# Optimization experiments

Measured on AMD Instinct MI355X. Metric: run time of the kernel, lower is better.

The kernel has to match this reference:

```python
import jax, jax.numpy as jnp
import numpy as np

D = 8
W = 256
NUM_FREQS = 10
NUM_FREQS_VIEWS = 4
SKIPS = (4,)
PE_DIM = 3 + 2 * 3 * NUM_FREQS        # 63
VE_DIM = 3 + 2 * 3 * NUM_FREQS_VIEWS  # 27
N_RAYS, N_SAMPLES = 4096, 64


def embed(x, num_freqs):
    # torch order: [x, sin(x*f0), cos(x*f0), sin(x*f1), cos(x*f1), ...]
    freqs = (2.0 ** jnp.arange(num_freqs)).astype(x.dtype)
    xf = x[..., None, :] * freqs[:, None]              # [..., F, 3]
    sc = jnp.stack([jnp.sin(xf), jnp.cos(xf)], axis=-2)  # [..., F, 2, 3]
    return jnp.concatenate([x, sc.reshape(*x.shape[:-1], num_freqs * 6)], -1)


def setup_inputs() -> dict:
    key = jax.random.key(0)
    ks = iter(jax.random.split(key, 32))
    inp = {}
    inp["input_pts"] = jax.random.normal(next(ks), (N_RAYS, N_SAMPLES, 3), jnp.float32)
    inp["input_views"] = jax.random.normal(next(ks), (N_RAYS, 3), jnp.float32)
    # pts MLP: layer 5 (index 5) takes W + PE_DIM due to skip after layer 4
    in_dims = [PE_DIM] + [(W + PE_DIM) if i in SKIPS else W for i in range(D - 1)]
    for i, d in enumerate(in_dims):
        inp[f"pts_w{i}"] = jax.random.normal(next(ks), (d, W), jnp.float32) / np.sqrt(d).astype(np.float32)
        inp[f"pts_b{i}"] = jnp.zeros((W,), jnp.float32)
    inp["views_w"] = jax.random.normal(next(ks), (VE_DIM + W, W // 2), jnp.float32) / np.sqrt(VE_DIM + W).astype(np.float32)
    inp["views_b"] = jnp.zeros((W // 2,), jnp.float32)
    inp["feat_w"] = jax.random.normal(next(ks), (W, W), jnp.float32) / np.sqrt(W).astype(np.float32)
    inp["feat_b"] = jnp.zeros((W,), jnp.float32)
    inp["alpha_w"] = jax.random.normal(next(ks), (W, 1), jnp.float32) / np.sqrt(W).astype(np.float32)
    inp["alpha_b"] = jnp.zeros((1,), jnp.float32)
    inp["rgb_w"] = jax.random.normal(next(ks), (W // 2, 3), jnp.float32) / np.sqrt(W // 2).astype(np.float32)
    inp["rgb_b"] = jnp.zeros((3,), jnp.float32)
    return inp


def reference(input_pts, input_views,
              pts_w0, pts_b0, pts_w1, pts_b1, pts_w2, pts_b2, pts_w3, pts_b3,
              pts_w4, pts_b4, pts_w5, pts_b5, pts_w6, pts_b6, pts_w7, pts_b7,
              views_w, views_b, feat_w, feat_b, alpha_w, alpha_b, rgb_w, rgb_b):
    pts_ws = [pts_w0, pts_w1, pts_w2, pts_w3, pts_w4, pts_w5, pts_w6, pts_w7]
    pts_bs = [pts_b0, pts_b1, pts_b2, pts_b3, pts_b4, pts_b5, pts_b6, pts_b7]
    R, S = input_pts.shape[0], input_pts.shape[1]
    ep = embed(input_pts, NUM_FREQS).reshape(-1, PE_DIM)            # [R*S, 63]
    ev = embed(input_views, NUM_FREQS_VIEWS)                        # [R, 27]
    ev = jnp.broadcast_to(ev[:, None, :], (R, S, VE_DIM)).reshape(-1, VE_DIM)
    h = ep
    for i in range(D):
        h = jax.nn.relu(h @ pts_ws[i] + pts_bs[i])
        if i in SKIPS:
            h = jnp.concatenate([ep, h], -1)
    alpha = h @ alpha_w + alpha_b                                    # [R*S, 1]
    feature = h @ feat_w + feat_b                                    # [R*S, W]
    h2 = jax.nn.relu(jnp.concatenate([feature, ev], -1) @ views_w + views_b)
    rgb = h2 @ rgb_w + rgb_b                                         # [R*S, 3]
    return jnp.concatenate([rgb, alpha], -1).reshape(R, S, 4)
```

## Files before the change

kernel.cpp:

```cpp
#include <hip/hip_runtime.h>

typedef _Float16 h16;
typedef __attribute__((ext_vector_type(8))) _Float16 half8;
typedef __attribute__((ext_vector_type(4))) _Float16 half4;
typedef __attribute__((ext_vector_type(4))) float f32x4;
typedef __attribute__((ext_vector_type(16))) float f32x16;

constexpr size_t OFF_P0 = 0;
constexpr size_t OFF_P1 = 16384;
constexpr size_t OFF_P2 = 81920;
constexpr size_t OFF_P3 = 147456;
constexpr size_t OFF_P4 = 212992;
constexpr size_t OFF_P5 = 278528;
constexpr size_t OFF_P6 = 360448;
constexpr size_t OFF_P7 = 425984;
constexpr size_t OFF_FEAT = 491520;
constexpr size_t OFF_VIEWS = 557056;

__device__ __forceinline__ f32x16 mfma32(half8 a, half8 b, f32x16 c) {
  return __builtin_amdgcn_mfma_f32_32x32x16_f16(a, b, c, 0, 0, 0);
}
__device__ __forceinline__ half8 ldfrag(const h16* __restrict__ base, int frag, int l) {
  return *(const half8*)(base + (size_t)frag * 512 + (size_t)l * 8);
}
__device__ __forceinline__ half8 ldsfrag(const h16* __restrict__ base, int frag, int l) {
  return *(const half8*)(base + frag * 512 + l * 8);
}

__global__ void convw_kernel(const float* __restrict__ src, h16* __restrict__ dst,
                             int Ksrc, int N, int Kp, int p, int npad, int rot) {
  int t = blockIdx.x * 256 + threadIdx.x;
  int nfrags = (Kp >> 4) * (N >> 5);
  int frag = t >> 6;
  if (frag >= nfrags) return;
  int l = t & 63;
  int ntiles = N >> 5;
  int kt = frag / ntiles;
  int nt = frag - kt * ntiles;
  int col = nt * 32 + (l & 31);
  int kbase = kt * 16 + (l >> 5) * 8;
  half8 v;
#pragma unroll
  for (int j = 0; j < 8; ++j) {
    int pr = kbase + j + rot;
    if (pr >= Kp) pr -= Kp;
    float x = 0.f;
    if (pr < p) {
      x = src[(size_t)pr * N + col];
    } else if (pr >= p + npad) {
      int r = pr - npad;
      if (r < Ksrc) x = src[(size_t)r * N + col];
    }
    v[j] = (h16)x;
  }
  *(half8*)(dst + (size_t)frag * 512 + (size_t)l * 8) = v;
}

struct Params {
  const float* pts;
  const float* views;
  const h16* wf;
  const float* pb[8];
  const float* views_b;
  const float* feat_b;
  const float* alpha_w;
  const float* alpha_b;
  const float* rgb_w;
  const float* rgb_b;
  float* out;
};

template <bool RELU>
__device__ __forceinline__ void epiW(h16* __restrict__ Y, const f32x16& A,
                                     int rt, int ct, const float* __restrict__ bias,
                                     int lr, int lh) {
#pragma unroll
  for (int g = 0; g < 4; ++g) {
    int col0 = ct * 32 + g * 8 + lh * 4;
    f32x4 bv = *(const f32x4*)(bias + col0);
    half4 pk;
#pragma unroll
    for (int i = 0; i < 4; ++i) {
      float v = A[g * 4 + i] + bv[i];
      if (RELU) v = fmaxf(v, 0.f);
      pk[i] = (h16)v;
    }
    *(half4*)(Y + (rt * 16 + ct * 2 + (g >> 1)) * 512 + ((g & 1) * 32 + lr) * 8 + lh * 4) = pk;
  }
}

template <int KTTOT, int XSTRIDE, bool RELU, bool EXTEP>
__device__ __forceinline__ void layerT(
    const h16* __restrict__ X, const h16* __restrict__ EPb, h16* __restrict__ Y,
    const h16* __restrict__ wcur, const h16* __restrict__ wnext,
    int nstride, int nbA, int nbB, const float* __restrict__ bias,
    half8 (&rA)[4], half8 (&rB)[4], int rp, int ctA, int ctB, int l) {
  const int lr = l & 31, lh = l >> 5;
  f32x16 a00 = (f32x16)0.f, a01 = (f32x16)0.f, a10 = (f32x16)0.f, a11 = (f32x16)0.f;
#pragma unroll
  for (int kt = 0; kt < KTTOT; ++kt) {
    half8 x0, x1;
    if (!EXTEP || kt < 16) {
      x0 = ldsfrag(X, (2 * rp) * XSTRIDE + kt, l);
      x1 = ldsfrag(X, (2 * rp + 1) * XSTRIDE + kt, l);
    } else {
      x0 = ldsfrag(EPb, (2 * rp) * 4 + (kt - 16), l);
      x1 = ldsfrag(EPb, (2 * rp + 1) * 4 + (kt - 16), l);
    }
    half8 bA = rA[kt & 3], bB = rB[kt & 3];
    if (kt + 4 < KTTOT) {
      rA[kt & 3] = ldfrag(wcur, (kt + 4) * 8 + ctA, l);
      rB[kt & 3] = ldfrag(wcur, (kt + 4) * 8 + ctB, l);
    } else {
      rA[kt & 3] = ldfrag(wnext, (kt + 4 - KTTOT) * nstride + nbA, l);
      rB[kt & 3] = ldfrag(wnext, (kt + 4 - KTTOT) * nstride + nbB, l);
    }
    a00 = mfma32(bA, x0, a00);
    a01 = mfma32(bB, x0, a01);
    a10 = mfma32(bA, x1, a10);
    a11 = mfma32(bB, x1, a11);
  }
  epiW<RELU>(Y, a00, 2 * rp, ctA, bias, lr, lh);
  epiW<RELU>(Y, a01, 2 * rp, ctB, bias, lr, lh);
  epiW<RELU>(Y, a10, 2 * rp + 1, ctA, bias, lr, lh);
  epiW<RELU>(Y, a11, 2 * rp + 1, ctB, bias, lr, lh);
  __syncthreads();
}

__global__ __launch_bounds__(512, 2) void nerf_kernel(Params P) {
  __shared__ __align__(16) h16 ep[16 * 512];
  __shared__ __align__(16) h16 h0[64 * 512];
  __shared__ __align__(16) h16 h1[64 * 512];
  __shared__ __align__(16) h16 evp[64];

  const int tid = threadIdx.x;
  const int w = tid >> 6, l = tid & 63;
  const int rp = w & 1, cp = w >> 1;
  const int ctA = 2 * cp, ctB = 2 * cp + 1;
  const h16* wf = P.wf;

  half8 rA[4], rB[4];
#pragma unroll
  for (int j = 0; j < 4; ++j) {
    rA[j] = ldfrag(wf + OFF_P0, j * 8 + ctA, l);
    rB[j] = ldfrag(wf + OFF_P0, j * 8 + ctB, l);
  }

  {
    const int s = tid >> 2, q = tid & 3;
    const float* ps = P.pts + ((size_t)blockIdx.x * 128 + s) * 3;
    const float x0 = ps[0], x1 = ps[1], x2 = ps[2];
    half8 v0, v1;
#pragma unroll
    for (int jj = 0; jj < 16; ++jj) {
      int p = q * 16 + jj;
      float val;
      if (p < 3) {
        val = p == 0 ? x0 : (p == 1 ? x1 : x2);
      } else if (p < 63) {
        int t = p - 3;
        int f = t / 6, rem = t % 6, d = rem % 3;
        float x = (d == 0 ? x0 : (d == 1 ? x1 : x2)) * (float)(1 << f);
        val = (rem < 3) ? sinf(x) : cosf(x);
      } else {
        val = 0.f;
      }
      if (jj < 8) v0[jj] = (h16)val; else v1[jj - 8] = (h16)val;
    }
    int fr = (s >> 5) * 4 + q;
    *(half8*)(ep + fr * 512 + (s & 31) * 8) = v0;
    *(half8*)(ep + fr * 512 + (32 + (s & 31)) * 8) = v1;
  }
  if (tid < 64) {
    const int r = tid >> 5, idx = tid & 31;
    float v = 0.f;
    if (idx < 27) {
      if (idx < 3) {
        v = P.views[((size_t)blockIdx.x * 2 + r) * 3 + idx];
      } else {
        const int f = (idx - 3) / 6, rem = (idx - 3) % 6, d = rem % 3;
        const float x = P.views[((size_t)blockIdx.x * 2 + r) * 3 + d] * (float)(1 << f);
        v = (rem < 3) ? sinf(x) : cosf(x);
      }
    }
    evp[r * 32 + idx] = (h16)v;
  }
  __syncthreads();

  layerT<4, 4, true, false>(ep, ep, h0, wf + OFF_P0, wf + OFF_P1, 8, ctA, ctB, P.pb[0], rA, rB, rp, ctA, ctB, l);
  layerT<16, 16, true, false>(h0, ep, h1, wf + OFF_P1, wf + OFF_P2, 8, ctA, ctB, P.pb[1], rA, rB, rp, ctA, ctB, l);
  layerT<16, 16, true, false>(h1, ep, h0, wf + OFF_P2, wf + OFF_P3, 8, ctA, ctB, P.pb[2], rA, rB, rp, ctA, ctB, l);
  layerT<16, 16, true, false>(h0, ep, h1, wf + OFF_P3, wf + OFF_P4, 8, ctA, ctB, P.pb[3], rA, rB, rp, ctA, ctB, l);
  layerT<16, 16, true, false>(h1, ep, h0, wf + OFF_P4, wf + OFF_P5, 8, ctA, ctB, P.pb[4], rA, rB, rp, ctA, ctB, l);
  layerT<20, 16, true, true>(h0, ep, h1, wf + OFF_P5, wf + OFF_P6, 8, ctA, ctB, P.pb[5], rA, rB, rp, ctA, ctB, l);
  layerT<16, 16, true, false>(h1, ep, h0, wf + OFF_P6, wf + OFF_P7, 8, ctA, ctB, P.pb[6], rA, rB, rp, ctA, ctB, l);
  layerT<16, 16, true, false>(h0, ep, h1, wf + OFF_P7, wf + OFF_FEAT, 8, ctA, ctB, P.pb[7], rA, rB, rp, ctA, ctB, l);

  float alpha_reg;
  {
    const int s = tid >> 2, q = tid & 3;
    float sum = 0.f;
#pragma unroll
    for (int j = 0; j < 8; ++j) {
      int k0 = q * 64 + j * 8;
      half8 hv = *(const half8*)(h1 + ((s >> 5) * 16 + (k0 >> 4)) * 512 +
                                 ((s & 31) + 32 * ((k0 >> 3) & 1)) * 8);
      f32x4 w0 = *(const f32x4*)(P.alpha_w + k0);
      f32x4 w1 = *(const f32x4*)(P.alpha_w + k0 + 4);
      sum += (float)hv[0] * w0[0] + (float)hv[1] * w0[1] + (float)hv[2] * w0[2] + (float)hv[3] * w0[3];
      sum += (float)hv[4] * w1[0] + (float)hv[5] * w1[1] + (float)hv[6] * w1[2] + (float)hv[7] * w1[3];
    }
    sum += __shfl_xor(sum, 1);
    sum += __shfl_xor(sum, 2);
    alpha_reg = sum + P.alpha_b[0];
  }

  layerT<16, 16, false, false>(h1, ep, h0, wf + OFF_FEAT, wf + OFF_VIEWS, 4,
                               2 * (w >> 2), 2 * (w >> 2) + 1, P.feat_b,
                               rA, rB, rp, ctA, ctB, l);

  {
    const int rt = w & 3, cv = w >> 2;
    const int vA = 2 * cv, vB = 2 * cv + 1;
    const int lr = l & 31, lh = l >> 5;
    const h16* wV = wf + OFF_VIEWS;
    f32x16 accA = (f32x16)0.f, accB = (f32x16)0.f;
#pragma unroll
    for (int kt = 0; kt < 18; ++kt) {
      half8 x;
      if (kt < 16) x = ldsfrag(h0, rt * 16 + kt, l);
      else x = *(const half8*)(evp + (rt >> 1) * 32 + (kt - 16) * 16 + lh * 8);
      half8 bA = rA[kt & 3], bB = rB[kt & 3];
      if (kt + 4 < 18) {
        rA[kt & 3] = ldfrag(wV, (kt + 4) * 4 + vA, l);
        rB[kt & 3] = ldfrag(wV, (kt + 4) * 4 + vB, l);
      }
      accA = mfma32(bA, x, accA);
      accB = mfma32(bB, x, accB);
    }
    epiW<true>(h1, accA, rt, vA, P.views_b, lr, lh);
    epiW<true>(h1, accB, rt, vB, P.views_b, lr, lh);
    __syncthreads();
  }

  {
    const int s = tid >> 2, q = tid & 3;
    float r0 = 0.f, r1 = 0.f, r2 = 0.f;
#pragma unroll
    for (int j = 0; j < 4; ++j) {
      int k0 = q * 32 + j * 8;
      half8 hv = *(const half8*)(h1 + ((s >> 5) * 16 + (k0 >> 4)) * 512 +
                                 ((s & 31) + 32 * ((k0 >> 3) & 1)) * 8);
#pragma unroll
      for (int i = 0; i < 8; ++i) {
        const float f = (float)hv[i];
        r0 += f * P.rgb_w[(k0 + i) * 3 + 0];
        r1 += f * P.rgb_w[(k0 + i) * 3 + 1];
        r2 += f * P.rgb_w[(k0 + i) * 3 + 2];
      }
    }
    r0 += __shfl_xor(r0, 1); r0 += __shfl_xor(r0, 2);
    r1 += __shfl_xor(r1, 1); r1 += __shfl_xor(r1, 2);
    r2 += __shfl_xor(r2, 1); r2 += __shfl_xor(r2, 2);
    if (q == 0) {
      float4 o;
      o.x = r0 + P.rgb_b[0];
      o.y = r1 + P.rgb_b[1];
      o.z = r2 + P.rgb_b[2];
      o.w = alpha_reg;
      *(float4*)(P.out + ((size_t)blockIdx.x * 128 + s) * 4) = o;
    }
  }
}

extern "C" void kernel_launch(void* const* d_in, const int* in_sizes, int n_in,
                              void* d_out, int out_size, void* d_ws, size_t ws_size,
                              hipStream_t stream) {
  h16* wsw = (h16*)d_ws;
  auto conv = [&](int idx, int Ksrc, int N, int Kp, int p, int npad, int rot, size_t off) {
    int nfrags = (Kp / 16) * (N / 32);
    int total = nfrags * 64;
    convw_kernel<<<(total + 255) / 256, 256, 0, stream>>>(
        (const float*)d_in[idx], wsw + off, Ksrc, N, Kp, p, npad, rot);
  };
  conv(2, 63, 256, 64, 63, 1, 0, OFF_P0);
  conv(4, 256, 256, 256, 256, 0, 0, OFF_P1);
  conv(6, 256, 256, 256, 256, 0, 0, OFF_P2);
  conv(8, 256, 256, 256, 256, 0, 0, OFF_P3);
  conv(10, 256, 256, 256, 256, 0, 0, OFF_P4);
  conv(12, 319, 256, 320, 63, 1, 64, OFF_P5);
  conv(14, 256, 256, 256, 256, 0, 0, OFF_P6);
  conv(16, 256, 256, 256, 256, 0, 0, OFF_P7);
  conv(20, 256, 256, 256, 256, 0, 0, OFF_FEAT);
  conv(18, 283, 128, 288, 283, 5, 0, OFF_VIEWS);

  Params P;
  P.pts = (const float*)d_in[0];
  P.views = (const float*)d_in[1];
  P.wf = wsw;
  for (int i = 0; i < 8; ++i) P.pb[i] = (const float*)d_in[3 + 2 * i];
  P.views_b = (const float*)d_in[19];
  P.feat_b = (const float*)d_in[21];
  P.alpha_w = (const float*)d_in[22];
  P.alpha_b = (const float*)d_in[23];
  P.rgb_w = (const float*)d_in[24];
  P.rgb_b = (const float*)d_in[25];
  P.out = (float*)d_out;

  nerf_kernel<<<2048, 512, 0, stream>>>(P);
}
```

Before: 432.9 us.

## Use 1024-thread blocks over 256 rows with a single in-place activation buffer

Each block now processes 256 sample rows with 16 waves, and each wave computes a 32-row by 128-column output tile. Weights fetched from global or L2 are therefore reused across twice as many rows per block. The ping-pong h0/h1 and ep shared buffers are merged into one in-place buffer, with an extra barrier before each epilogue writes back. The positional embedding is kept in registers for the skip layer. The cross-layer register prefetch of weight fragments is dropped, so global load latency may be less well hidden behind the MFMAs.

After: 854.9 us. 1.97x slower.

```diff
diff --git a/kernel.cpp b/kernel.cpp
--- a/kernel.cpp
+++ b/kernel.cpp
@@ -89,121 +89,132 @@
   }
 }
 
-template <int KTTOT, int XSTRIDE, bool RELU, bool EXTEP>
-__device__ __forceinline__ void layerT(
-    const h16* __restrict__ X, const h16* __restrict__ EPb, h16* __restrict__ Y,
-    const h16* __restrict__ wcur, const h16* __restrict__ wnext,
-    int nstride, int nbA, int nbB, const float* __restrict__ bias,
-    half8 (&rA)[4], half8 (&rB)[4], int rp, int ctA, int ctB, int l) {
-  const int lr = l & 31, lh = l >> 5;
-  f32x16 a00 = (f32x16)0.f, a01 = (f32x16)0.f, a10 = (f32x16)0.f, a11 = (f32x16)0.f;
-#pragma unroll
-  for (int kt = 0; kt < KTTOT; ++kt) {
-    half8 x0, x1;
-    if (!EXTEP || kt < 16) {
-      x0 = ldsfrag(X, (2 * rp) * XSTRIDE + kt, l);
-      x1 = ldsfrag(X, (2 * rp + 1) * XSTRIDE + kt, l);
-    } else {
-      x0 = ldsfrag(EPb, (2 * rp) * 4 + (kt - 16), l);
-      x1 = ldsfrag(EPb, (2 * rp + 1) * 4 + (kt - 16), l);
-    }
-    half8 bA = rA[kt & 3], bB = rB[kt & 3];
-    if (kt + 4 < KTTOT) {
-      rA[kt & 3] = ldfrag(wcur, (kt + 4) * 8 + ctA, l);
-      rB[kt & 3] = ldfrag(wcur, (kt + 4) * 8 + ctB, l);
-    } else {
-      rA[kt & 3] = ldfrag(wnext, (kt + 4 - KTTOT) * nstride + nbA, l);
-      rB[kt & 3] = ldfrag(wnext, (kt + 4 - KTTOT) * nstride + nbB, l);
-    }
-    a00 = mfma32(bA, x0, a00);
-    a01 = mfma32(bB, x0, a01);
-    a10 = mfma32(bA, x1, a10);
-    a11 = mfma32(bB, x1, a11);
-  }
-  epiW<RELU>(Y, a00, 2 * rp, ctA, bias, lr, lh);
-  epiW<RELU>(Y, a01, 2 * rp, ctB, bias, lr, lh);
-  epiW<RELU>(Y, a10, 2 * rp + 1, ctA, bias, lr, lh);
-  epiW<RELU>(Y, a11, 2 * rp + 1, ctB, bias, lr, lh);
+__device__ __forceinline__ float embed_col(int c, float x0, float x1, float x2) {
+  if (c < 3) return c == 0 ? x0 : (c == 1 ? x1 : x2);
+  if (c >= 63) return 0.f;
+  int t = c - 3;
+  int f = t / 6, rem = t - f * 6;
+  int d = rem >= 3 ? rem - 3 : rem;
+  float x = (d == 0 ? x0 : (d == 1 ? x1 : x2)) * (float)(1 << f);
+  return (rem < 3) ? sinf(x) : cosf(x);
+}
+
+template <bool RELU, bool EXTEP>
+__device__ __forceinline__ void layerT(h16* __restrict__ h,
+                                       const h16* __restrict__ wcur,
+                                       const float* __restrict__ bias,
+                                       const half8* epf,
+                                       int rt, int ct0, int l, int lr, int lh) {
+  f32x16 a0 = (f32x16)0.f, a1 = (f32x16)0.f, a2 = (f32x16)0.f, a3 = (f32x16)0.f;
+#pragma unroll
+  for (int kt = 0; kt < 16; ++kt) {
+    half8 x = ldsfrag(h, rt * 16 + kt, l);
+    half8 w0 = ldfrag(wcur, kt * 8 + ct0 + 0, l);
+    half8 w1 = ldfrag(wcur, kt * 8 + ct0 + 1, l);
+    half8 w2 = ldfrag(wcur, kt * 8 + ct0 + 2, l);
+    half8 w3 = ldfrag(wcur, kt * 8 + ct0 + 3, l);
+    a0 = mfma32(w0, x, a0);
+    a1 = mfma32(w1, x, a1);
+    a2 = mfma32(w2, x, a2);
+    a3 = mfma32(w3, x, a3);
+  }
+  if (EXTEP) {
+#pragma unroll
+    for (int j = 0; j < 4; ++j) {
+      half8 x = epf[j];
+      half8 w0 = ldfrag(wcur, (16 + j) * 8 + ct0 + 0, l);
+      half8 w1 = ldfrag(wcur, (16 + j) * 8 + ct0 + 1, l);
+      half8 w2 = ldfrag(wcur, (16 + j) * 8 + ct0 + 2, l);
+      half8 w3 = ldfrag(wcur, (16 + j) * 8 + ct0 + 3, l);
+      a0 = mfma32(w0, x, a0);
+      a1 = mfma32(w1, x, a1);
+      a2 = mfma32(w2, x, a2);
+      a3 = mfma32(w3, x, a3);
+    }
+  }
   __syncthreads();
-}
-
-__global__ __launch_bounds__(512, 2) void nerf_kernel(Params P) {
-  __shared__ __align__(16) h16 ep[16 * 512];
-  __shared__ __align__(16) h16 h0[64 * 512];
-  __shared__ __align__(16) h16 h1[64 * 512];
-  __shared__ __align__(16) h16 evp[64];
+  epiW<RELU>(h, a0, rt, ct0 + 0, bias, lr, lh);
+  epiW<RELU>(h, a1, rt, ct0 + 1, bias, lr, lh);
+  epiW<RELU>(h, a2, rt, ct0 + 2, bias, lr, lh);
+  epiW<RELU>(h, a3, rt, ct0 + 3, bias, lr, lh);
+  __syncthreads();
+}
+
+__global__ __launch_bounds__(1024, 4) void nerf_kernel(Params P) {
+  __shared__ __align__(16) h16 h[128 * 512];
+  __shared__ __align__(16) h16 evp[128];
+  __shared__ float alpha_s[256];
 
   const int tid = threadIdx.x;
   const int w = tid >> 6, l = tid & 63;
-  const int rp = w & 1, cp = w >> 1;
-  const int ctA = 2 * cp, ctB = 2 * cp + 1;
+  const int lr = l & 31, lh = l >> 5;
+  const int rt = w & 7, ch = w >> 3;
+  const int ct0 = ch * 4;
   const h16* wf = P.wf;
-
-  half8 rA[4], rB[4];
-#pragma unroll
-  for (int j = 0; j < 4; ++j) {
-    rA[j] = ldfrag(wf + OFF_P0, j * 8 + ctA, l);
-    rB[j] = ldfrag(wf + OFF_P0, j * 8 + ctB, l);
-  }
-
-  {
-    const int s = tid >> 2, q = tid & 3;
-    const float* ps = P.pts + ((size_t)blockIdx.x * 128 + s) * 3;
-    const float x0 = ps[0], x1 = ps[1], x2 = ps[2];
-    half8 v0, v1;
-#pragma unroll
-    for (int jj = 0; jj < 16; ++jj) {
-      int p = q * 16 + jj;
-      float val;
-      if (p < 3) {
-        val = p == 0 ? x0 : (p == 1 ? x1 : x2);
-      } else if (p < 63) {
-        int t = p - 3;
-        int f = t / 6, rem = t % 6, d = rem % 3;
-        float x = (d == 0 ? x0 : (d == 1 ? x1 : x2)) * (float)(1 << f);
-        val = (rem < 3) ? sinf(x) : cosf(x);
-      } else {
-        val = 0.f;
-      }
-      if (jj < 8) v0[jj] = (h16)val; else v1[jj - 8] = (h16)val;
-    }
-    int fr = (s >> 5) * 4 + q;
-    *(half8*)(ep + fr * 512 + (s & 31) * 8) = v0;
-    *(half8*)(ep + fr * 512 + (32 + (s & 31)) * 8) = v1;
-  }
-  if (tid < 64) {
+  const size_t row_base = (size_t)blockIdx.x * 256;
+
+  const float* ps = P.pts + (row_base + rt * 32 + lr) * 3;
+  const float x0 = ps[0], x1 = ps[1], x2 = ps[2];
+  half8 epf[4];
+#pragma unroll
+  for (int kt = 0; kt < 4; ++kt) {
+    half8 v;
+#pragma unroll
+    for (int j = 0; j < 8; ++j)
+      v[j] = (h16)embed_col(kt * 16 + lh * 8 + j, x0, x1, x2);
+    epf[kt] = v;
+  }
+  if (tid < 128) {
     const int r = tid >> 5, idx = tid & 31;
     float v = 0.f;
     if (idx < 27) {
       if (idx < 3) {
-        v = P.views[((size_t)blockIdx.x * 2 + r) * 3 + idx];
+        v = P.views[((size_t)blockIdx.x * 4 + r) * 3 + idx];
       } else {
         const int f = (idx - 3) / 6, rem = (idx - 3) % 6, d = rem % 3;
-        const float x = P.views[((size_t)blockIdx.x * 2 + r) * 3 + d] * (float)(1 << f);
+        const float x = P.views[((size_t)blockIdx.x * 4 + r) * 3 + d] * (float)(1 << f);
         v = (rem < 3) ? sinf(x) : cosf(x);
       }
     }
-    evp[r * 32 + idx] = (h16)v;
-  }
-  __syncthreads();
-
-  layerT<4, 4, true, false>(ep, ep, h0, wf + OFF_P0, wf + OFF_P1, 8, ctA, ctB, P.pb[0], rA, rB, rp, ctA, ctB, l);
-  layerT<16, 16, true, false>(h0, ep, h1, wf + OFF_P1, wf + OFF_P2, 8, ctA, ctB, P.pb[1], rA, rB, rp, ctA, ctB, l);
-  layerT<16, 16, true, false>(h1, ep, h0, wf + OFF_P2, wf + OFF_P3, 8, ctA, ctB, P.pb[2], rA, rB, rp, ctA, ctB, l);
-  layerT<16, 16, true, false>(h0, ep, h1, wf + OFF_P3, wf + OFF_P4, 8, ctA, ctB, P.pb[3], rA, rB, rp, ctA, ctB, l);
-  layerT<16, 16, true, false>(h1, ep, h0, wf + OFF_P4, wf + OFF_P5, 8, ctA, ctB, P.pb[4], rA, rB, rp, ctA, ctB, l);
-  layerT<20, 16, true, true>(h0, ep, h1, wf + OFF_P5, wf + OFF_P6, 8, ctA, ctB, P.pb[5], rA, rB, rp, ctA, ctB, l);
-  layerT<16, 16, true, false>(h1, ep, h0, wf + OFF_P6, wf + OFF_P7, 8, ctA, ctB, P.pb[6], rA, rB, rp, ctA, ctB, l);
-  layerT<16, 16, true, false>(h0, ep, h1, wf + OFF_P7, wf + OFF_FEAT, 8, ctA, ctB, P.pb[7], rA, rB, rp, ctA, ctB, l);
-
-  float alpha_reg;
+    evp[tid] = (h16)v;
+  }
+
+  {
+    f32x16 a0 = (f32x16)0.f, a1 = (f32x16)0.f, a2 = (f32x16)0.f, a3 = (f32x16)0.f;
+#pragma unroll
+    for (int kt = 0; kt < 4; ++kt) {
+      half8 x = epf[kt];
+      half8 w0 = ldfrag(wf + OFF_P0, kt * 8 + ct0 + 0, l);
+      half8 w1 = ldfrag(wf + OFF_P0, kt * 8 + ct0 + 1, l);
+      half8 w2 = ldfrag(wf + OFF_P0, kt * 8 + ct0 + 2, l);
+      half8 w3 = ldfrag(wf + OFF_P0, kt * 8 + ct0 + 3, l);
+      a0 = mfma32(w0, x, a0);
+      a1 = mfma32(w1, x, a1);
+      a2 = mfma32(w2, x, a2);
+      a3 = mfma32(w3, x, a3);
+    }
+    epiW<true>(h, a0, rt, ct0 + 0, P.pb[0], lr, lh);
+    epiW<true>(h, a1, rt, ct0 + 1, P.pb[0], lr, lh);
+    epiW<true>(h, a2, rt, ct0 + 2, P.pb[0], lr, lh);
+    epiW<true>(h, a3, rt, ct0 + 3, P.pb[0], lr, lh);
+    __syncthreads();
+  }
+
+  layerT<true, false>(h, wf + OFF_P1, P.pb[1], epf, rt, ct0, l, lr, lh);
+  layerT<true, false>(h, wf + OFF_P2, P.pb[2], epf, rt, ct0, l, lr, lh);
+  layerT<true, false>(h, wf + OFF_P3, P.pb[3], epf, rt, ct0, l, lr, lh);
+  layerT<true, false>(h, wf + OFF_P4, P.pb[4], epf, rt, ct0, l, lr, lh);
+  layerT<true, true>(h, wf + OFF_P5, P.pb[5], epf, rt, ct0, l, lr, lh);
+  layerT<true, false>(h, wf + OFF_P6, P.pb[6], epf, rt, ct0, l, lr, lh);
+  layerT<true, false>(h, wf + OFF_P7, P.pb[7], epf, rt, ct0, l, lr, lh);
+
   {
     const int s = tid >> 2, q = tid & 3;
     float sum = 0.f;
 #pragma unroll
     for (int j = 0; j < 8; ++j) {
       int k0 = q * 64 + j * 8;
-      half8 hv = *(const half8*)(h1 + ((s >> 5) * 16 + (k0 >> 4)) * 512 +
+      half8 hv = *(const half8*)(h + ((s >> 5) * 16 + (k0 >> 4)) * 512 +
                                  ((s & 31) + 32 * ((k0 >> 3) & 1)) * 8);
       f32x4 w0 = *(const f32x4*)(P.alpha_w + k0);
       f32x4 w1 = *(const f32x4*)(P.alpha_w + k0 + 4);
@@ -212,34 +223,34 @@
     }
     sum += __shfl_xor(sum, 1);
     sum += __shfl_xor(sum, 2);
-    alpha_reg = sum + P.alpha_b[0];
-  }
-
-  layerT<16, 16, false, false>(h1, ep, h0, wf + OFF_FEAT, wf + OFF_VIEWS, 4,
-                               2 * (w >> 2), 2 * (w >> 2) + 1, P.feat_b,
-                               rA, rB, rp, ctA, ctB, l);
+    if (q == 0) alpha_s[s] = sum + P.alpha_b[0];
+  }
+
+  layerT<false, false>(h, wf + OFF_FEAT, P.feat_b, epf, rt, ct0, l, lr, lh);
 
   {
-    const int rt = w & 3, cv = w >> 2;
-    const int vA = 2 * cv, vB = 2 * cv + 1;
-    const int lr = l & 31, lh = l >> 5;
+    const int cv0 = ch * 2;
     const h16* wV = wf + OFF_VIEWS;
-    f32x16 accA = (f32x16)0.f, accB = (f32x16)0.f;
-#pragma unroll
-    for (int kt = 0; kt < 18; ++kt) {
-      half8 x;
-      if (kt < 16) x = ldsfrag(h0, rt * 16 + kt, l);
-      else x = *(const half8*)(evp + (rt >> 1) * 32 + (kt - 16) * 16 + lh * 8);
-      half8 bA = rA[kt & 3], bB = rB[kt & 3];
-      if (kt + 4 < 18) {
-        rA[kt & 3] = ldfrag(wV, (kt + 4) * 4 + vA, l);
-        rB[kt & 3] = ldfrag(wV, (kt + 4) * 4 + vB, l);
-      }
-      accA = mfma32(bA, x, accA);
-      accB = mfma32(bB, x, accB);
-    }
-    epiW<true>(h1, accA, rt, vA, P.views_b, lr, lh);
-    epiW<true>(h1, accB, rt, vB, P.views_b, lr, lh);
+    f32x16 b0 = (f32x16)0.f, b1 = (f32x16)0.f;
+#pragma unroll
+    for (int kt = 0; kt < 16; ++kt) {
+      half8 x = ldsfrag(h, rt * 16 + kt, l);
+      half8 w0 = ldfrag(wV, kt * 4 + cv0 + 0, l);
+      half8 w1 = ldfrag(wV, kt * 4 + cv0 + 1, l);
+      b0 = mfma32(w0, x, b0);
+      b1 = mfma32(w1, x, b1);
+    }
+#pragma unroll
+    for (int kt = 16; kt < 18; ++kt) {
+      half8 x = *(const half8*)(evp + (rt >> 1) * 32 + (kt - 16) * 16 + lh * 8);
+      half8 w0 = ldfrag(wV, kt * 4 + cv0 + 0, l);
+      half8 w1 = ldfrag(wV, kt * 4 + cv0 + 1, l);
+      b0 = mfma32(w0, x, b0);
+      b1 = mfma32(w1, x, b1);
+    }
+    __syncthreads();
+    epiW<true>(h, b0, rt, cv0 + 0, P.views_b, lr, lh);
+    epiW<true>(h, b1, rt, cv0 + 1, P.views_b, lr, lh);
     __syncthreads();
   }
 
@@ -249,7 +260,7 @@
 #pragma unroll
     for (int j = 0; j < 4; ++j) {
       int k0 = q * 32 + j * 8;
-      half8 hv = *(const half8*)(h1 + ((s >> 5) * 16 + (k0 >> 4)) * 512 +
+      half8 hv = *(const half8*)(h + ((s >> 5) * 16 + (k0 >> 4)) * 512 +
                                  ((s & 31) + 32 * ((k0 >> 3) & 1)) * 8);
 #pragma unroll
       for (int i = 0; i < 8; ++i) {
@@ -267,8 +278,8 @@
       o.x = r0 + P.rgb_b[0];
       o.y = r1 + P.rgb_b[1];
       o.z = r2 + P.rgb_b[2];
-      o.w = alpha_reg;
-      *(float4*)(P.out + ((size_t)blockIdx.x * 128 + s) * 4) = o;
+      o.w = alpha_s[s];
+      *(float4*)(P.out + (row_base + s) * 4) = o;
     }
   }
 }
@@ -307,5 +318,5 @@
   P.rgb_b = (const float*)d_in[25];
   P.out = (float*)d_out;
 
-  nerf_kernel<<<2048, 512, 0, stream>>>(P);
-}
+  nerf_kernel<<<1024, 1024, 0, stream>>>(P);
+}
```
